# Performance work log

Hardware: AMD Instinct MI355X
Metric: run time of the kernel (lower is better)

## Reference

```python
import jax, jax.numpy as jnp
import numpy as np

N = 20000      # nodes per type
E = 320000     # edges per relation
F = 512        # raw feature dim
H = 4          # attention heads
C = 128        # hidden_channels per head
B = 64         # batch_size (num graphs)
HH = H * C
INNER = 64
NEG_SLOPE = 0.2


def _gatv2(x_src, x_dst, ei, Wl, Wr, att, b):
    """PyG GATv2Conv (concat=True, add_self_loops=True, neg_slope=0.2).
    x_src:[Ns,Fin] x_dst:[Nd,Fin'] ei:[2,E] Wl,Wr:[Fin,H*C] att:[H,C] b:[H*C].
    Returns [Nd, H*C]. Self-loop edges appended (inputs assumed loop-free)."""
    n_dst = x_dst.shape[0]
    loop = jnp.arange(min(x_src.shape[0], n_dst), dtype=ei.dtype)
    src = jnp.concatenate([ei[0], loop])
    dst = jnp.concatenate([ei[1], loop])
    xl = (x_src @ Wl).reshape(-1, H, C)   # source-side transform
    xr = (x_dst @ Wr).reshape(-1, H, C)   # target-side transform
    e = jax.nn.leaky_relu(xl[src] + xr[dst], NEG_SLOPE)   # [E',H,C]
    logit = jnp.einsum('ehc,hc->eh', e, att)               # [E',H]
    m = jax.ops.segment_max(logit, dst, num_segments=n_dst)
    m = jnp.where(jnp.isfinite(m), m, 0.0)
    p = jnp.exp(logit - m[dst])
    s = jax.ops.segment_sum(p, dst, num_segments=n_dst)
    alpha = p / jnp.maximum(s[dst], 1e-16)                 # per-dst softmax
    out = jax.ops.segment_sum(alpha[:, :, None] * xl[src], dst, num_segments=n_dst)
    return out.reshape(n_dst, HH) + b


def _layer(x_i, x_j, ei_ii, ei_jj, ei_ij, ei_ji, Wl, Wr, att, b):
    # relation order: 0:(x_i->x_i) 1:(x_j->x_j) 2:(x_i->x_j) 3:(x_j->x_i); HeteroConv aggr='sum'
    oi = _gatv2(x_i, x_i, ei_ii, Wl[0], Wr[0], att[0], b[0]) \
       + _gatv2(x_j, x_i, ei_ji, Wl[3], Wr[3], att[3], b[3])
    oj = _gatv2(x_j, x_j, ei_jj, Wl[1], Wr[1], att[1], b[1]) \
       + _gatv2(x_i, x_j, ei_ij, Wl[2], Wr[2], att[2], b[2])
    # head-sum + tanh: x.view(-1, heads, hidden).sum(1).tanh()
    oi = jnp.tanh(oi.reshape(-1, H, C).sum(axis=1))
    oj = jnp.tanh(oj.reshape(-1, H, C).sum(axis=1))
    return oi, oj


def setup_inputs() -> dict:
    key = jax.random.key(0)
    ks = jax.random.split(key, 24)
    inp = {
        'x_i': jax.random.normal(ks[0], (N, F), jnp.float32),
        'x_j': jax.random.normal(ks[1], (N, F), jnp.float32),
        'ei_ii': jax.random.randint(ks[2], (2, E), 0, N, jnp.int32),
        'ei_jj': jax.random.randint(ks[3], (2, E), 0, N, jnp.int32),
        'ei_ij': jax.random.randint(ks[4], (2, E), 0, N, jnp.int32),
        'ei_ji': jax.random.randint(ks[5], (2, E), 0, N, jnp.int32),
        'batch_i': jnp.sort(jax.random.randint(ks[6], (N,), 0, B, jnp.int32)),
        'batch_j': jnp.sort(jax.random.randint(ks[7], (N,), 0, B, jnp.int32)),
        'Wl0': jax.random.normal(ks[8], (4, F, HH), jnp.float32) / np.sqrt(F),
        'Wr0': jax.random.normal(ks[9], (4, F, HH), jnp.float32) / np.sqrt(F),
        'att0': jax.random.normal(ks[10], (4, H, C), jnp.float32) / np.sqrt(C),
        'b0': jnp.zeros((4, HH), jnp.float32),
        'Wl1': jax.random.normal(ks[11], (4, C, HH), jnp.float32) / np.sqrt(C),
        'Wr1': jax.random.normal(ks[12], (4, C, HH), jnp.float32) / np.sqrt(C),
        'att1': jax.random.normal(ks[13], (4, H, C), jnp.float32) / np.sqrt(C),
        'b1': jnp.zeros((4, HH), jnp.float32),
        'W_out': jax.random.normal(ks[14], (C, 1), jnp.float32) / np.sqrt(C),
        'b_out': jnp.zeros((1,), jnp.float32),
        'W_i': jax.random.normal(ks[15], (C, INNER), jnp.float32) / np.sqrt(C),
        'b_i': jnp.zeros((INNER,), jnp.float32),
        'W_j': jax.random.normal(ks[16], (C, INNER), jnp.float32) / np.sqrt(C),
        'b_j': jnp.zeros((INNER,), jnp.float32),
    }
    return inp


def reference(x_i, x_j, ei_ii, ei_jj, ei_ij, ei_ji, batch_i, batch_j,
              Wl0, Wr0, att0, b0, Wl1, Wr1, att1, b1,
              W_out, b_out, W_i, b_i, W_j, b_j):
    x_i, x_j = _layer(x_i, x_j, ei_ii, ei_jj, ei_ij, ei_ji, Wl0, Wr0, att0, b0)
    x_i, x_j = _layer(x_i, x_j, ei_ii, ei_jj, ei_ij, ei_ji, Wl1, Wr1, att1, b1)
    # global_add_pool per graph, then unsqueeze(1) + tanh
    p_i = jnp.tanh(jax.ops.segment_sum(x_i, batch_i, num_segments=B))[:, None, :]  # [B,1,C]
    p_j = jnp.tanh(jax.ops.segment_sum(x_j, batch_j, num_segments=B))[:, None, :]
    y_i = p_i @ W_i + b_i   # [B,1,INNER]
    y_j = p_j @ W_j + b_j
    x = (p_i + p_j)[:, 0, :]            # cat along dim=1 then sum(dim=1)
    logits = jax.nn.sigmoid(x @ W_out + b_out)   # [B,1]
    return (logits, y_i, y_j)
```

## Files before the change

kernel.cpp:

```cpp
#include <hip/hip_runtime.h>

#define NN      20000
#define EE      320000
#define ETOT    340000
#define FD      512
#define HH_     4
#define CD      128
#define HHD     512
#define BG      64
#define INNERD  64

typedef __attribute__((ext_vector_type(8))) short bf16x8;
typedef __attribute__((ext_vector_type(4))) float f32x4;

__device__ __forceinline__ float bf2f(unsigned v) { return __uint_as_float(v << 16); }
__device__ __forceinline__ unsigned short f2bf(float f) {
    unsigned u = __float_as_uint(f);
    unsigned r = 0x7fffu + ((u >> 16) & 1u);
    return (unsigned short)((u + r) >> 16);
}
__device__ __forceinline__ void load8bf(const unsigned short* p, float* f) {
    uint4 u = *reinterpret_cast<const uint4*>(p);
    f[0] = bf2f(u.x & 0xffffu); f[1] = bf2f(u.x >> 16);
    f[2] = bf2f(u.y & 0xffffu); f[3] = bf2f(u.y >> 16);
// ... 39 lines not shown
        part[t] += v;
        __syncthreads();
    }
    int run = (t > 0) ? part[t - 1] : 0;
    #pragma unroll
    for (int i = 0; i < 20; ++i) {
        int n = base + i;
        if (n < NN) { rowptr[n] = run; cursor[n] = run; run += cnt[n] + 1; }
    }
    if (t == 1023) rowptr[NN] = run;
}

__global__ __launch_bounds__(256) void csr_scatter16(const int* __restrict__ ei,
                                                     int* __restrict__ cursor,
                                                     unsigned short* __restrict__ srcs) {
    int idx = blockIdx.x * blockDim.x + threadIdx.x;
    if (idx >= ETOT) return;
    int src, dst;
    if (idx < EE) { src = ei[idx]; dst = ei[EE + idx]; }
    else          { src = dst = idx - EE; }
    int pos = atomicAdd(&cursor[dst], 1);
    srcs[pos] = (unsigned short)src;
}

__global__ __launch_bounds__(256) void csr_hist4(
    const int* __restrict__ e0, const int* __restrict__ e1,
    const int* __restrict__ e2, const int* __restrict__ e3,
    int* __restrict__ cnt)
{
    int idx = blockIdx.x * blockDim.x + threadIdx.x;
    if (idx >= 4 * EE) return;
    int r = idx / EE, e = idx - r * EE;
    const int* ei = r == 0 ? e0 : r == 1 ? e1 : r == 2 ? e2 : e3;
    atomicAdd(&cnt[r * NN + ei[EE + e]], 1);
}

__global__ __launch_bounds__(1024) void csr_scan4(const int* __restrict__ cnt_all,
                                                  int* __restrict__ rowptr_all,
                                                  int* __restrict__ cursor_all)
{
    const int r = blockIdx.x;
    const int* cnt = cnt_all + r * NN;
    int* rowptr = rowptr_all + r * (NN + 4);
    int* cursor = cursor_all + r * NN;
    __shared__ int part[1024];
    int t = threadIdx.x;
    int base = t * 20;
    int s = 0;
    #pragma unroll
    for (int i = 0; i < 20; ++i) { int n = base + i; if (n < NN) s += cnt[n] + 1; }
    part[t] = s;
    __syncthreads();
    for (int off = 1; off < 1024; off <<= 1) {
        int v = (t >= off) ? part[t - off] : 0;
        __syncthreads();
        part[t] += v;
        __syncthreads();
    }
    int run = (t > 0) ? part[t - 1] : 0;
    #pragma unroll
    for (int i = 0; i < 20; ++i) {
        int n = base + i;
        if (n < NN) { rowptr[n] = run; cursor[n] = run; run += cnt[n] + 1; }
    }
    if (t == 1023) rowptr[NN] = run;
}

__global__ __launch_bounds__(256) void csr_scatter4(
    const int* __restrict__ e0, const int* __restrict__ e1,
    const int* __restrict__ e2, const int* __restrict__ e3,
    int* __restrict__ cursor_all, unsigned short* __restrict__ srcs_all)
{
    int idx = blockIdx.x * blockDim.x + threadIdx.x;
    if (idx >= 4 * ETOT) return;
    int r = idx / ETOT, t = idx - r * ETOT;
    const int* ei = r == 0 ? e0 : r == 1 ? e1 : r == 2 ? e2 : e3;
    int src, dst;
    if (t < EE) { src = ei[t]; dst = ei[EE + t]; }
    else        { src = dst = t - EE; }
    int pos = atomicAdd(&cursor_all[r * NN + dst], 1);
    srcs_all[(size_t)r * ETOT + pos] = (unsigned short)src;
}

__global__ __launch_bounds__(256) void wsplit_t(const float* __restrict__ W,
                                                unsigned short* __restrict__ Whi,
                                                unsigned short* __restrict__ Wlo,
                                                int K)
{
    __shared__ float tile[64][65];
    const int nt = 512 / 64;
    const int kt = K / 64;
    int bid = blockIdx.x;
    int in = bid % nt; int ik = (bid / nt) % kt; int r = bid / (nt * kt);
    int t = threadIdx.x;
    const float* Wr_ = W + (size_t)r * K * 512;
    #pragma unroll
    for (int rep = 0; rep < 16; ++rep) {
        int idx = rep * 256 + t;
        int kk = idx >> 6, nn = idx & 63;
        tile[kk][nn] = Wr_[(size_t)(ik * 64 + kk) * 512 + in * 64 + nn];
    }
    __syncthreads();
    #pragma unroll
    for (int rep = 0; rep < 16; ++rep) {
        int idx = rep * 256 + t;
        int nn = idx >> 6, kk = idx & 63;
        unsigned short h, l; split_f32(tile[kk][nn], h, l);
        int n = in * 64 + nn;
        int k = ik * 64 + kk;
        size_t o = (size_t)r * 512 * K + ((size_t)(k >> 5) * 512 + n) * 32 + (k & 31);
        Whi[o] = h; Wlo[o] = l;
    }
}

template <typename TA, bool A_EXACT>
__device__ __forceinline__ void gemm_body(
    const TA* __restrict__ A, const unsigned short* __restrict__ Bhg,
    const unsigned short* __restrict__ Blg, unsigned short* __restrict__ C,
    int bx, int by, int M, int K, int N)
{
    __shared__ unsigned short Ah[128][40];
    __shared__ unsigned short Al[A_EXACT ? 1 : 128][40];

    const int tid = threadIdx.x;
    const int wave = tid >> 6, lane = tid & 63;
    const int quad = lane >> 4, lrow = lane & 15;
    const int wr = (wave >> 1) * 64, wc = (wave & 1) * 64;
    const int tileM = by * 128, tileN = bx * 128;

    const int srow = tid >> 1;
    const int sks  = (tid & 1) * 16;
    const int sgm  = tileM + srow;

    const size_t bfrag = ((size_t)(tileN + wc + lrow) << 5) + quad * 8;
    const size_t kblk  = (size_t)N << 5;

    f32x4 acc[4][4] = {};

    for (int k0 = 0; k0 < K; k0 += 32) {
        if constexpr (!A_EXACT) {
            bf16x8 ph[2] = {{}, {}}, pl[2] = {{}, {}};
            if (sgm < M) {
                const float* Ap = (const float*)A + (size_t)sgm * K + k0 + sks;
                #pragma unroll
                for (int s = 0; s < 2; ++s) {
                    float4 f0 = reinterpret_cast<const float4*>(Ap)[2 * s];
                    float4 f1 = reinterpret_cast<const float4*>(Ap)[2 * s + 1];
                    float xv[8] = {f0.x, f0.y, f0.z, f0.w, f1.x, f1.y, f1.z, f1.w};
                    #pragma unroll
                    for (int pp = 0; pp < 4; ++pp) {
                        unsigned u0 = __float_as_uint(xv[2 * pp]);
                        unsigned u1 = __float_as_uint(xv[2 * pp + 1]);
                        reinterpret_cast<unsigned*>(&ph[s])[pp] =
                            __builtin_amdgcn_perm(u1, u0, 0x07060302u);
                        float r0 = xv[2 * pp]     - __uint_as_float(u0 & 0xffff0000u);
                        float r1 = xv[2 * pp + 1] - __uint_as_float(u1 & 0xffff0000u);
                        reinterpret_cast<unsigned*>(&pl[s])[pp] =
                            __builtin_amdgcn_perm(__float_as_uint(r1), __float_as_uint(r0), 0x07060302u);
                    }
                }
            }
            *reinterpret_cast<bf16x8*>(&Ah[srow][sks])     = ph[0];
            *reinterpret_cast<bf16x8*>(&Ah[srow][sks + 8]) = ph[1];
            *reinterpret_cast<bf16x8*>(&Al[srow][sks])     = pl[0];
            *reinterpret_cast<bf16x8*>(&Al[srow][sks + 8]) = pl[1];
        } else {
            bf16x8 v0 = {}, v1 = {};
            if (sgm < M) {
                const unsigned short* Ap = (const unsigned short*)A + (size_t)sgm * K + k0 + sks;
                v0 = reinterpret_cast<const bf16x8*>(Ap)[0];
                v1 = reinterpret_cast<const bf16x8*>(Ap)[1];
            }
            *reinterpret_cast<bf16x8*>(&Ah[srow][sks])     = v0;
            *reinterpret_cast<bf16x8*>(&Ah[srow][sks + 8]) = v1;
        }
        bf16x8 bh[4], bl[4];
        {
            const unsigned short* Bb = Bhg + (size_t)(k0 >> 5) * kblk + bfrag;
            const unsigned short* Bc = Blg + (size_t)(k0 >> 5) * kblk + bfrag;
            #pragma unroll
            for (int ni = 0; ni < 4; ++ni) {
                bh[ni] = *reinterpret_cast<const bf16x8*>(Bb + ((size_t)ni << 9));
                bl[ni] = *reinterpret_cast<const bf16x8*>(Bc + ((size_t)ni << 9));
            }
        }
        __syncthreads();
        bf16x8 ah[4], al[4];
        #pragma unroll
        for (int mi = 0; mi < 4; ++mi) {
            ah[mi] = *reinterpret_cast<const bf16x8*>(&Ah[wr + mi * 16 + lrow][quad * 8]);
            if constexpr (!A_EXACT)
                al[mi] = *reinterpret_cast<const bf16x8*>(&Al[wr + mi * 16 + lrow][quad * 8]);
        }
        #pragma unroll
        for (int mi = 0; mi < 4; ++mi)
// ... 445 lines not shown
        size_t ai = (size_t)dst * CD + lane * 8;
        if (add_in) {
            #pragma unroll
            for (int j = 0; j < 8; ++j) o[j] += acc[ai + j];
        }
        if (fin_mode == 0) {
            #pragma unroll
            for (int j = 0; j < 8; ++j) acc[ai + j] = o[j];
        } else {
            int c0 = lane * 8;
            #pragma unroll
            for (int j = 0; j < 8; ++j) {
                float bb = 0.f;
                #pragma unroll
                for (int h = 0; h < HH_; ++h)
                    bb += bA[h * CD + c0 + j] + bB[h * CD + c0 + j];
                o[j] = tanhf(o[j] + bb);
            }
            if (fin_mode == 1) {
                #pragma unroll
                for (int j = 0; j < 8; ++j) z[ai + j] = f2bf(o[j]);
            } else {
                #pragma unroll
                for (int j = 0; j < 8; ++j) acc[ai + j] = o[j];
            }
        }
    }
}

__global__ __launch_bounds__(256) void fused_aggr4d(
    const int* __restrict__ rp0, const unsigned short* __restrict__ sr0,
    const unsigned short* __restrict__ xl0, const unsigned short* __restrict__ xr0,
    const float* __restrict__ attA,
    const int* __restrict__ rp1, const unsigned short* __restrict__ sr1,
    const unsigned short* __restrict__ xl1, const unsigned short* __restrict__ xr1,
    const float* __restrict__ attB,
    float* __restrict__ acc, int fin_mode,
    const float* __restrict__ bA, const float* __restrict__ bB,
    unsigned short* __restrict__ z,
    const int* __restrict__ batch, float* __restrict__ pool)
{
    int dst = (int)((blockIdx.x * (size_t)blockDim.x + threadIdx.x) >> 6);
    int lane = threadIdx.x & 63;
    if (dst >= NN) return;
    aggr4d_body(dst, lane, rp0, sr0, xl0, xr0, attA, rp1, sr1, xl1, xr1, attB,
                acc, fin_mode, bA, bB, z);
}

__global__ __launch_bounds__(256) void fused_aggr4d_pair(
    const int* __restrict__ irp0, const unsigned short* __restrict__ isr0,
    const unsigned short* __restrict__ ixl0, const unsigned short* __restrict__ ixr0,
    const float* __restrict__ iattA,
    const int* __restrict__ irp1, const unsigned short* __restrict__ isr1,
    const unsigned short* __restrict__ ixl1, const unsigned short* __restrict__ ixr1,
    const float* __restrict__ iattB,
    float* __restrict__ accA,
    const float* __restrict__ ibA, const float* __restrict__ ibB,
    const int* __restrict__ jrp0, const unsigned short* __restrict__ jsr0,
    const unsigned short* __restrict__ jxl0, const unsigned short* __restrict__ jxr0,
    const float* __restrict__ jattA,
    const int* __restrict__ jrp1, const unsigned short* __restrict__ jsr1,
    const unsigned short* __restrict__ jxl1, const unsigned short* __restrict__ jxr1,
    const float* __restrict__ jattB,
    float* __restrict__ accB,
    const float* __restrict__ jbA, const float* __restrict__ jbB)
{
    const int half = NN / 4;
    int lane = threadIdx.x & 63;
    if ((int)blockIdx.x < half) {
        int dst = (int)((blockIdx.x * (size_t)blockDim.x + threadIdx.x) >> 6);
        if (dst >= NN) return;
        aggr4d_body(dst, lane, irp0, isr0, ixl0, ixr0, iattA,
                    irp1, isr1, ixl1, ixr1, iattB, accA, 2, ibA, ibB, nullptr);
    } else {
        int dst = (int)(((blockIdx.x - half) * (size_t)blockDim.x + threadIdx.x) >> 6);
        if (dst >= NN) return;
        aggr4d_body(dst, lane, jrp0, jsr0, jxl0, jxr0, jattA,
                    jrp1, jsr1, jxl1, jxr1, jattB, accB, 2, jbA, jbB, nullptr);
    }
}

template <typename TA, bool A_EXACT>
__global__ __launch_bounds__(256, 3) void gemm_aggr_fused(
    int ngemm,
    const TA* __restrict__ A0, const TA* __restrict__ A1,
    const TA* __restrict__ A2, const TA* __restrict__ A3,
    const unsigned short* __restrict__ B0h, const unsigned short* __restrict__ B0l,
    const unsigned short* __restrict__ B1h, const unsigned short* __restrict__ B1l,
    const unsigned short* __restrict__ B2h, const unsigned short* __restrict__ B2l,
    const unsigned short* __restrict__ B3h, const unsigned short* __restrict__ B3l,
    unsigned short* __restrict__ C0, unsigned short* __restrict__ C1,
    unsigned short* __restrict__ C2, unsigned short* __restrict__ C3,
    int M, int K, int N,
    const int* __restrict__ rp0, const unsigned short* __restrict__ sr0,
    const unsigned short* __restrict__ xl0, const unsigned short* __restrict__ xr0,
    const float* __restrict__ attA,
    const int* __restrict__ rp1, const unsigned short* __restrict__ sr1,
    const unsigned short* __restrict__ xl1, const unsigned short* __restrict__ xr1,
    const float* __restrict__ attB,
    float* __restrict__ acc, int fin_mode,
    const float* __restrict__ bA, const float* __restrict__ bB,
    unsigned short* __restrict__ zout)
{
    if ((int)blockIdx.x < ngemm) {
        int b = blockIdx.x;
        int xcd = b & 7, q8 = ngemm >> 3, r8 = ngemm & 7;
        int work = (xcd < r8 ? xcd * (q8 + 1) : r8 * (q8 + 1) + (xcd - r8) * q8) + (b >> 3);
        const int gx = N / 128, gy = (M + 127) / 128;
        int bx = work % gx; int t2 = work / gx; int by = t2 % gy; int bz = t2 / gy;
        const TA* A = bz == 0 ? A0 : bz == 1 ? A1 : bz == 2 ? A2 : A3;
        const unsigned short* Bh = bz == 0 ? B0h : bz == 1 ? B1h : bz == 2 ? B2h : B3h;
        const unsigned short* Bl = bz == 0 ? B0l : bz == 1 ? B1l : bz == 2 ? B2l : B3l;
        unsigned short* C = bz == 0 ? C0 : bz == 1 ? C1 : bz == 2 ? C2 : C3;
        gemm_body<TA, A_EXACT>(A, Bh, Bl, C, bx, by, M, K, N);
    } else {
        int dst = (int)(((blockIdx.x - ngemm) * (size_t)blockDim.x + threadIdx.x) >> 6);
        int lane = threadIdx.x & 63;
        if (dst >= NN) return;
        aggr4d_body(dst, lane, rp0, sr0, xl0, xr0, attA, rp1, sr1, xl1, xr1, attB,
                    acc, fin_mode, bA, bB, zout);
    }
}

__global__ __launch_bounds__(512) void pool_reduce(
    const float* __restrict__ acc, const int* __restrict__ batch,
    float* __restrict__ pool)
{
    int b = blockIdx.x;
    int t = threadIdx.x & (CD - 1);
    int q = threadIdx.x >> 7;
    int lo, hi;
    { int l = 0, r = NN; while (l < r) { int m = (l + r) >> 1; if (batch[m] < b) l = m + 1; else r = m; } lo = l; }
    { int l = lo, r = NN; while (l < r) { int m = (l + r) >> 1; if (batch[m] <= b) l = m + 1; else r = m; } hi = l; }
    float s = 0.f;
    for (int nrow = lo + q; nrow < hi; nrow += 4)
        s += acc[(size_t)nrow * CD + t];
    __shared__ float red[4][CD];
    red[q][t] = s;
    __syncthreads();
    if (q == 0)
        pool[(size_t)b * CD + t] = red[0][t] + red[1][t] + red[2][t] + red[3][t];
}

__global__ __launch_bounds__(512) void pool_reduce2(
    const float* __restrict__ accA, const int* __restrict__ batchA, float* __restrict__ poolA,
    const float* __restrict__ accB, const int* __restrict__ batchB, float* __restrict__ poolB)
{
    int g = blockIdx.x;
    const float* acc = (g < BG) ? accA : accB;
    const int* batch = (g < BG) ? batchA : batchB;
    float* pool = (g < BG) ? poolA : poolB;
    int b = (g < BG) ? g : g - BG;
    int t = threadIdx.x & (CD - 1);
    int q = threadIdx.x >> 7;
    int lo, hi;
    { int l = 0, r = NN; while (l < r) { int m = (l + r) >> 1; if (batch[m] < b) l = m + 1; else r = m; } lo = l; }
    { int l = lo, r = NN; while (l < r) { int m = (l + r) >> 1; if (batch[m] <= b) l = m + 1; else r = m; } hi = l; }
    float s = 0.f;
    for (int nrow = lo + q; nrow < hi; nrow += 4)
        s += acc[(size_t)nrow * CD + t];
    __shared__ float red[4][CD];
    red[q][t] = s;
    __syncthreads();
    if (q == 0)
        pool[(size_t)b * CD + t] = red[0][t] + red[1][t] + red[2][t] + red[3][t];
}

__global__ __launch_bounds__(128) void head_kernel(
    const float* __restrict__ pool_i, const float* __restrict__ pool_j,
    const float* __restrict__ W_out, const float* __restrict__ b_out,
    const float* __restrict__ W_i, const float* __restrict__ b_i,
    const float* __restrict__ W_j, const float* __restrict__ b_j,
    float* __restrict__ out)
{
    int b = blockIdx.x;
    int t = threadIdx.x;
    __shared__ float pi[CD], pj[CD];
    pi[t] = tanhf(pool_i[(size_t)b * CD + t]);
    pj[t] = tanhf(pool_j[(size_t)b * CD + t]);
    __syncthreads();
    if (t < INNERD) {
        float a = b_i[t];
        for (int c = 0; c < CD; ++c) a += pi[c] * W_i[c * INNERD + t];
        out[BG + (size_t)b * INNERD + t] = a;
    } else {
        int k = t - INNERD;
        float a = b_j[k];
        for (int c = 0; c < CD; ++c) a += pj[c] * W_j[c * INNERD + k];
        out[BG + BG * INNERD + (size_t)b * INNERD + k] = a;
    }
    if (t == 0) {
        float a = b_out[0];
        for (int c = 0; c < CD; ++c) a += (pi[c] + pj[c]) * W_out[c];
        out[b] = 1.f / (1.f + expf(-a));
    }
}

struct Ws {
    unsigned short *xl, *xr, *xl2, *xr2, *xl3, *xr3, *xl4, *xr4, *z_i, *z_j;
// ... 140 lines not shown
    const int* batch_j = (const int*)d_in[7];
    const float* Wl0   = (const float*)d_in[8];
    const float* Wr0   = (const float*)d_in[9];
    const float* att0  = (const float*)d_in[10];
    const float* b0    = (const float*)d_in[11];
    const float* Wl1   = (const float*)d_in[12];
    const float* Wr1   = (const float*)d_in[13];
    const float* att1  = (const float*)d_in[14];
    const float* b1    = (const float*)d_in[15];
    const float* W_out = (const float*)d_in[16];
    const float* b_out = (const float*)d_in[17];
    const float* W_i   = (const float*)d_in[18];
    const float* b_i   = (const float*)d_in[19];
    const float* W_j   = (const float*)d_in[20];
    const float* b_j   = (const float*)d_in[21];
    float* out = (float*)d_out;

    const size_t FAT2_BYTES = (size_t)NN * HHD * 2 * 2 + (size_t)NN * CD * 4
                            + (size_t)NN * CD * 2 * 2 + 4 * (size_t)ETOT * 2
                            + 4 * (size_t)(NN + 4) * 4 + 4 * (size_t)NN * 4 * 2
                            + (size_t)BG * CD * 4 * 2;
    const size_t FAT1_BYTES = (size_t)NN * HHD * 2 * 2 + (size_t)NN * CD * 4
                            + (size_t)NN * CD * 2 * 2 + (size_t)ETOT * 2
                            + (size_t)(NN + 4) * 4 + (size_t)NN * 4 * 2
                            + (size_t)BG * CD * 4 * 2;
    const size_t WT0_ONE = (size_t)4 * 512 * 512 * 2;
    const size_t WT1_ONE = (size_t)4 * 512 * 128 * 2;
    const size_t WT_BYTES = 4 * WT0_ONE + 4 * WT1_ONE;
    const size_t X2_BYTES = 2 * (size_t)NN * HHD * 2;
    const size_t ACC2_BYTES = (size_t)NN * CD * 4;

    const int ncsr = (ws_size >= FAT2_BYTES) ? 4 : 1;
    const bool fat = (ws_size >= FAT1_BYTES);
    const bool fat_t = (ws_size >= FAT2_BYTES + WT_BYTES);
    const bool fat_m = (ws_size >= FAT2_BYTES + WT_BYTES + X2_BYTES);
    const bool fat_f = (ws_size >= FAT2_BYTES + WT_BYTES + 3 * X2_BYTES);
    const bool fat_g = (ws_size >= FAT2_BYTES + WT_BYTES + 3 * X2_BYTES + ACC2_BYTES);

    Ws w;
    char* p = (char*)d_ws;
    size_t xbytes = fat ? (size_t)NN * HHD * 2 : (size_t)NN * CD * 2;
    w.xl     = (unsigned short*)p; p += xbytes;
    w.xr     = (unsigned short*)p; p += xbytes;
    w.acc    = (float*)p;          p += (size_t)NN * CD * 4;
    w.z_i    = (unsigned short*)p; p += (size_t)NN * CD * 2;
    w.z_j    = (unsigned short*)p; p += (size_t)NN * CD * 2;
    {
        int* rowptr_all = (int*)p;            p += (size_t)ncsr * (NN + 4) * 4;
        unsigned short* srcs_all = (unsigned short*)p; p += (size_t)ncsr * ETOT * 2;
        for (int r = 0; r < 4; ++r) {
            int rr = (r < ncsr) ? r : 0;
            w.rowptr[r] = rowptr_all + (size_t)rr * (NN + 4);
            w.srcs[r]   = srcs_all + (size_t)rr * ETOT;
        }
    }
    w.cnt    = (int*)p;            p += (size_t)ncsr * NN * 4;
    w.cursor = (int*)p;            p += (size_t)ncsr * NN * 4;
    w.pool_i = (float*)p;          p += (size_t)BG * CD * 4;
    w.pool_j = (float*)p;          p += (size_t)BG * CD * 4;
    if (fat_t) {
        w.wt0l_h = (unsigned short*)p; p += WT0_ONE;
        w.wt0l_l = (unsigned short*)p; p += WT0_ONE;
        w.wt0r_h = (unsigned short*)p; p += WT0_ONE;
        w.wt0r_l = (unsigned short*)p; p += WT0_ONE;
        w.wt1l_h = (unsigned short*)p; p += WT1_ONE;
        w.wt1l_l = (unsigned short*)p; p += WT1_ONE;
        w.wt1r_h = (unsigned short*)p; p += WT1_ONE;
        w.wt1r_l = (unsigned short*)p; p += WT1_ONE;
    }
    if (fat_m) {
        w.xl2 = (unsigned short*)p; p += (size_t)NN * HHD * 2;
        w.xr2 = (unsigned short*)p; p += (size_t)NN * HHD * 2;
    }
    if (fat_f) {
        w.xl3 = (unsigned short*)p; p += (size_t)NN * HHD * 2;
        w.xr3 = (unsigned short*)p; p += (size_t)NN * HHD * 2;
        w.xl4 = (unsigned short*)p; p += (size_t)NN * HHD * 2;
        w.xr4 = (unsigned short*)p; p += (size_t)NN * HHD * 2;
    }
    if (fat_g) {
        w.acc2 = (float*)p; p += ACC2_BYTES;
    }

    hipMemsetAsync(w.pool_i, 0, (size_t)BG * CD * sizeof(float), stream);
    hipMemsetAsync(w.pool_j, 0, (size_t)BG * CD * sizeof(float), stream);

    const int* eis_all[4] = { ei_ii, ei_jj, ei_ij, ei_ji };
    const float* srcA0_i[2] = { x_i, x_j };  const float* dstA0_i[2] = { x_i, x_i };
    const float* srcA0_j[2] = { x_j, x_i };  const float* dstA0_j[2] = { x_j, x_j };
    const int rids_i[2] = { 0, 3 };
    const int rids_j[2] = { 1, 2 };
    const unsigned short* srcA1_i[2] = { w.z_i, w.z_j };
    const unsigned short* dstA1_i[2] = { w.z_i, w.z_i };
    const unsigned short* srcA1_j[2] = { w.z_j, w.z_i };
    const unsigned short* dstA1_j[2] = { w.z_j, w.z_j };

    if (fat_t) {
        hipMemsetAsync(w.cnt, 0, 4 * NN * sizeof(int), stream);
        csr_hist4<<<(4 * EE + 255) / 256, 256, 0, stream>>>(
            ei_ii, ei_jj, ei_ij, ei_ji, w.cnt);
        csr_scan4<<<4, 1024, 0, stream>>>(w.cnt, w.rowptr[0], w.cursor);
        csr_scatter4<<<(4 * ETOT + 255) / 256, 256, 0, stream>>>(
            ei_ii, ei_jj, ei_ij, ei_ji, w.cursor, w.srcs[0]);
        wsplit_t<<<4 * (FD / 64) * 8, 256, 0, stream>>>(Wl0, w.wt0l_h, w.wt0l_l, FD);
        wsplit_t<<<4 * (FD / 64) * 8, 256, 0, stream>>>(Wr0, w.wt0r_h, w.wt0r_l, FD);
        wsplit_t<<<4 * (CD / 64) * 8, 256, 0, stream>>>(Wl1, w.wt1l_h, w.wt1l_l, CD);
        wsplit_t<<<4 * (CD / 64) * 8, 256, 0, stream>>>(Wr1, w.wt1r_h, w.wt1r_l, CD);

        const int* rp_i[2] = { w.rowptr[0], w.rowptr[3] };
        const unsigned short* sr_i[2] = { w.srcs[0], w.srcs[3] };
        const int* rp_j[2] = { w.rowptr[1], w.rowptr[2] };
        const unsigned short* sr_j[2] = { w.srcs[1], w.srcs[2] };

        if (fat_g) {
            const size_t o0 = (size_t)0 * HHD * FD, o3 = (size_t)3 * HHD * FD;
            const size_t o1 = (size_t)1 * HHD * FD, o2 = (size_t)2 * HHD * FD;
            const size_t p0 = (size_t)0 * HHD * CD, p1 = (size_t)1 * HHD * CD;
            const size_t p2 = (size_t)2 * HHD * CD, p3 = (size_t)3 * HHD * CD;
            dim3 gg(HHD / 128, (NN + 127) / 128, 4);
            gemm_mfma_t4<float, false><<<gg, 256, 0, stream>>>(
                x_i, x_i, x_j, x_i,
                w.wt0l_h + o0, w.wt0l_l + o0, w.wt0r_h + o0, w.wt0r_l + o0,
                w.wt0l_h + o3, w.wt0l_l + o3, w.wt0r_h + o3, w.wt0r_l + o3,
                w.xl, w.xr, w.xl2, w.xr2, NN, FD, HHD);
            const int ngemm0 = (HHD / 128) * ((NN + 127) / 128) * 4;
            gemm_aggr_fused<float, false><<<ngemm0 + NN / 4, 256, 0, stream>>>(
                ngemm0,
                x_j, x_j, x_i, x_j,
                w.wt0l_h + o1, w.wt0l_l + o1, w.wt0r_h + o1, w.wt0r_l + o1,
                w.wt0l_h + o2, w.wt0l_l + o2, w.wt0r_h + o2, w.wt0r_l + o2,
                w.xl3, w.xr3, w.xl4, w.xr4, NN, FD, HHD,
                w.rowptr[0], w.srcs[0], w.xl, w.xr, att0 + (size_t)0 * HHD,
                w.rowptr[3], w.srcs[3], w.xl2, w.xr2, att0 + (size_t)3 * HHD,
                w.acc, 1, b0 + (size_t)0 * HHD, b0 + (size_t)3 * HHD, w.z_i);
            gemm_aggr_fused<unsigned short, true><<<ngemm0 + NN / 4, 256, 0, stream>>>(
                ngemm0,
                w.z_i, w.z_i, w.z_i, w.z_i,
                w.wt1l_h + p0, w.wt1l_l + p0, w.wt1r_h + p0, w.wt1r_l + p0,
                w.wt1r_h + p3, w.wt1r_l + p3, w.wt1l_h + p2, w.wt1l_l + p2,
                w.xl, w.xr, w.xr2, w.xl2, NN, CD, HHD,
                w.rowptr[1], w.srcs[1], w.xl3, w.xr3, att0 + (size_t)1 * HHD,
                w.rowptr[2], w.srcs[2], w.xl4, w.xr4, att0 + (size_t)2 * HHD,
                w.acc, 1, b0 + (size_t)1 * HHD, b0 + (size_t)2 * HHD, w.z_j);
            gemm_mfma_t4<unsigned short, true><<<gg, 256, 0, stream>>>(
                w.z_j, w.z_j, w.z_j, w.z_j,
                w.wt1l_h + p3, w.wt1l_l + p3, w.wt1l_h + p1, w.wt1l_l + p1,
                w.wt1r_h + p1, w.wt1r_l + p1, w.wt1r_h + p2, w.wt1r_l + p2,
                w.xl4, w.xl3, w.xr3, w.xr4, NN, CD, HHD);
            fused_aggr4d_pair<<<2 * (NN / 4), 256, 0, stream>>>(
                w.rowptr[0], w.srcs[0], w.xl, w.xr, att1 + (size_t)0 * HHD,
                w.rowptr[3], w.srcs[3], w.xl4, w.xr2, att1 + (size_t)3 * HHD,
                w.acc, b1 + (size_t)0 * HHD, b1 + (size_t)3 * HHD,
                w.rowptr[1], w.srcs[1], w.xl3, w.xr3, att1 + (size_t)1 * HHD,
                w.rowptr[2], w.srcs[2], w.xl2, w.xr4, att1 + (size_t)2 * HHD,
                w.acc2, b1 + (size_t)1 * HHD, b1 + (size_t)2 * HHD);
            pool_reduce2<<<2 * BG, 512, 0, stream>>>(
                w.acc, batch_i, w.pool_i, w.acc2, batch_j, w.pool_j);
        } else if (fat_f) {
            const size_t o0 = (size_t)0 * HHD * FD, o3 = (size_t)3 * HHD * FD;
            const size_t o1 = (size_t)1 * HHD * FD, o2 = (size_t)2 * HHD * FD;
            dim3 gg(HHD / 128, (NN + 127) / 128, 4);
            gemm_mfma_t4<float, false><<<gg, 256, 0, stream>>>(
                x_i, x_i, x_j, x_i,
                w.wt0l_h + o0, w.wt0l_l + o0, w.wt0r_h + o0, w.wt0r_l + o0,
                w.wt0l_h + o3, w.wt0l_l + o3, w.wt0r_h + o3, w.wt0r_l + o3,
                w.xl, w.xr, w.xl2, w.xr2, NN, FD, HHD);
            const int ngemm = (HHD / 128) * ((NN + 127) / 128) * 4;
            gemm_aggr_fused<float, false><<<ngemm + NN / 4, 256, 0, stream>>>(
                ngemm,
                x_j, x_j, x_i, x_j,
                w.wt0l_h + o1, w.wt0l_l + o1, w.wt0r_h + o1, w.wt0r_l + o1,
                w.wt0l_h + o2, w.wt0l_l + o2, w.wt0r_h + o2, w.wt0r_l + o2,
                w.xl3, w.xr3, w.xl4, w.xr4, NN, FD, HHD,
                w.rowptr[0], w.srcs[0], w.xl, w.xr, att0 + (size_t)0 * HHD,
                w.rowptr[3], w.srcs[3], w.xl2, w.xr2, att0 + (size_t)3 * HHD,
                w.acc, 1, b0 + (size_t)0 * HHD, b0 + (size_t)3 * HHD, w.z_i);
            fused_aggr4d<<<NN / 4, 256, 0, stream>>>(
                w.rowptr[1], w.srcs[1], w.xl3, w.xr3, att0 + (size_t)1 * HHD,
                w.rowptr[2], w.srcs[2], w.xl4, w.xr4, att0 + (size_t)2 * HHD,
                w.acc, 1, b0 + (size_t)1 * HHD, b0 + (size_t)2 * HHD,
                w.z_j, nullptr, nullptr);
            dim3 g8(HHD / 128, (NN + 127) / 128, 8);
            gemm_mfma_L1x8<<<g8, 256, 0, stream>>>(
                w.z_i, w.z_j, w.wt1l_h, w.wt1l_l, w.wt1r_h, w.wt1r_l,
                w.xl, w.xr, w.xl2, w.xr2, w.xl3, w.xr3, w.xl4, w.xr4,
                NN, CD, HHD);
            fused_aggr4d<<<NN / 4, 256, 0, stream>>>(
                w.rowptr[0], w.srcs[0], w.xl, w.xr, att1 + (size_t)0 * HHD,
                w.rowptr[3], w.srcs[3], w.xl2, w.xr2, att1 + (size_t)3 * HHD,
                w.acc, 2, b1 + (size_t)0 * HHD, b1 + (size_t)3 * HHD,
                nullptr, nullptr, nullptr);
            pool_reduce<<<BG, 512, 0, stream>>>(w.acc, batch_i, w.pool_i);
            fused_aggr4d<<<NN / 4, 256, 0, stream>>>(
                w.rowptr[1], w.srcs[1], w.xl3, w.xr3, att1 + (size_t)1 * HHD,
                w.rowptr[2], w.srcs[2], w.xl4, w.xr4, att1 + (size_t)2 * HHD,
                w.acc, 2, b1 + (size_t)1 * HHD, b1 + (size_t)2 * HHD,
                nullptr, nullptr, nullptr);
            pool_reduce<<<BG, 512, 0, stream>>>(w.acc, batch_j, w.pool_j);
        } else if (fat_m) {
            run_group_fat_m<float, false>(srcA0_i, dstA0_i, rp_i, sr_i, rids_i, FD,
                                          w.wt0l_h, w.wt0l_l, w.wt0r_h, w.wt0r_l,
                                          att0, b0, 1, w.z_i, nullptr, nullptr, w, stream);
            run_group_fat_m<float, false>(srcA0_j, dstA0_j, rp_j, sr_j, rids_j, FD,
                                          w.wt0l_h, w.wt0l_l, w.wt0r_h, w.wt0r_l,
                                          att0, b0, 1, w.z_j, nullptr, nullptr, w, stream);
            run_group_fat_m<unsigned short, true>(srcA1_i, dstA1_i, rp_i, sr_i, rids_i, CD,
                                                  w.wt1l_h, w.wt1l_l, w.wt1r_h, w.wt1r_l,
                                                  att1, b1, 2, nullptr, batch_i, w.pool_i, w, stream);
            pool_reduce<<<BG, 512, 0, stream>>>(w.acc, batch_i, w.pool_i);
            run_group_fat_m<unsigned short, true>(srcA1_j, dstA1_j, rp_j, sr_j, rids_j, CD,
                                                  w.wt1l_h, w.wt1l_l, w.wt1r_h, w.wt1r_l,
                                                  att1, b1, 2, nullptr, batch_j, w.pool_j, w, stream);
            pool_reduce<<<BG, 512, 0, stream>>>(w.acc, batch_j, w.pool_j);
        } else {
            run_group_fat_t<float, false>(srcA0_i, dstA0_i, rp_i, sr_i, rids_i, FD,
                                          w.wt0l_h, w.wt0l_l, w.wt0r_h, w.wt0r_l,
                                          att0, b0, 1, w.z_i, nullptr, nullptr, w, stream);
            run_group_fat_t<float, false>(srcA0_j, dstA0_j, rp_j, sr_j, rids_j, FD,
                                          w.wt0l_h, w.wt0l_l, w.wt0r_h, w.wt0r_l,
                                          att0, b0, 1, w.z_j, nullptr, nullptr, w, stream);
            run_group_fat_t<unsigned short, true>(srcA1_i, dstA1_i, rp_i, sr_i, rids_i, CD,
                                                  w.wt1l_h, w.wt1l_l, w.wt1r_h, w.wt1r_l,
                                                  att1, b1, 2, nullptr, batch_i, w.pool_i, w, stream);
            pool_reduce<<<BG, 512, 0, stream>>>(w.acc, batch_i, w.pool_i);
            run_group_fat_t<unsigned short, true>(srcA1_j, dstA1_j, rp_j, sr_j, rids_j, CD,
                                                  w.wt1l_h, w.wt1l_l, w.wt1r_h, w.wt1r_l,
                                                  att1, b1, 2, nullptr, batch_j, w.pool_j, w, stream);
            pool_reduce<<<BG, 512, 0, stream>>>(w.acc, batch_j, w.pool_j);
        }
    } else if (fat) {
        if (ncsr == 4) {
            for (int r = 0; r < 4; ++r)
                build_csr(eis_all[r], w.rowptr[r], w.srcs[r], w.cnt, w.cursor, stream);
            const int* rp_i[2] = { w.rowptr[0], w.rowptr[3] };
            const unsigned short* sr_i[2] = { w.srcs[0], w.srcs[3] };
            const int* rp_j[2] = { w.rowptr[1], w.rowptr[2] };
            const unsigned short* sr_j[2] = { w.srcs[1], w.srcs[2] };
            run_group_fat<float, false>(srcA0_i, dstA0_i, rp_i, sr_i, rids_i, FD,
                                        Wl0, Wr0, att0, b0, 1, w.z_i, nullptr, nullptr, w, stream);
            run_group_fat<float, false>(srcA0_j, dstA0_j, rp_j, sr_j, rids_j, FD,
                                        Wl0, Wr0, att0, b0, 1, w.z_j, nullptr, nullptr, w, stream);
            run_group_fat<unsigned short, true>(srcA1_i, dstA1_i, rp_i, sr_i, rids_i, CD,
                                                Wl1, Wr1, att1, b1, 2, nullptr, batch_i, w.pool_i, w, stream);
            pool_reduce<<<BG, 512, 0, stream>>>(w.acc, batch_i, w.pool_i);
            run_group_fat<unsigned short, true>(srcA1_j, dstA1_j, rp_j, sr_j, rids_j, CD,
                                                Wl1, Wr1, att1, b1, 2, nullptr, batch_j, w.pool_j, w, stream);
            pool_reduce<<<BG, 512, 0, stream>>>(w.acc, batch_j, w.pool_j);
        } else {
            for (int pass = 0; pass < 4; ++pass) {
                const int* rids = (pass & 1) ? rids_j : rids_i;
                for (int q = 0; q < 2; ++q) {
                    int r = rids[q];
// ... 50 lines not shown
```

Baseline: 1.237 ms.

## Interleave GEMM and aggregation blocks in fused kernel; merge weight-split launches

The fused GEMM+aggregation kernel now spreads GEMM tiles evenly across the block index range instead of putting all GEMM blocks first. Each block decides its role from a proportional mapping, so aggregation and GEMM blocks are co-resident and compute-bound and memory-bound work can overlap. The four weight-split launches are merged into one kernel, and the pool memsets are skipped on the fat path, where they appear to be unused. The interleaving may change cache locality and the XCD-aware tile assignment for the GEMM blocks.

Result: no change. 1.249 ms (+0.9%).

```diff
diff --git a/kernel.cpp b/kernel.cpp
--- a/kernel.cpp
+++ b/kernel.cpp
@@ -145,16 +145,14 @@
     srcs_all[(size_t)r * ETOT + pos] = (unsigned short)src;
 }
 
-__global__ __launch_bounds__(256) void wsplit_t(const float* __restrict__ W,
-                                                unsigned short* __restrict__ Whi,
-                                                unsigned short* __restrict__ Wlo,
-                                                int K)
+__device__ __forceinline__ void wsplit_body(const float* __restrict__ W,
+                                            unsigned short* __restrict__ Whi,
+                                            unsigned short* __restrict__ Wlo,
+                                            int K, int bid)
 {
     __shared__ float tile[64][65];
     const int nt = 512 / 64;
-    const int kt = K / 64;
-    int bid = blockIdx.x;
-    int in = bid % nt; int ik = (bid / nt) % kt; int r = bid / (nt * kt);
+    int in = bid % nt; int ik = (bid / nt) % (K / 64); int r = bid / (nt * (K / 64));
     int t = threadIdx.x;
     const float* Wr_ = W + (size_t)r * K * 512;
     #pragma unroll
@@ -174,6 +172,21 @@
         size_t o = (size_t)r * 512 * K + ((size_t)(k >> 5) * 512 + n) * 32 + (k & 31);
         Whi[o] = h; Wlo[o] = l;
     }
+}
+
+__global__ __launch_bounds__(256) void wsplit_all(
+    const float* __restrict__ Wl0, const float* __restrict__ Wr0,
+    const float* __restrict__ Wl1, const float* __restrict__ Wr1,
+    unsigned short* __restrict__ w0lh, unsigned short* __restrict__ w0ll,
+    unsigned short* __restrict__ w0rh, unsigned short* __restrict__ w0rl,
+    unsigned short* __restrict__ w1lh, unsigned short* __restrict__ w1ll,
+    unsigned short* __restrict__ w1rh, unsigned short* __restrict__ w1rl)
+{
+    int b = blockIdx.x;
+    if (b < 256)      wsplit_body(Wl0, w0lh, w0ll, FD, b);
+    else if (b < 512) wsplit_body(Wr0, w0rh, w0rl, FD, b - 256);
+    else if (b < 576) wsplit_body(Wl1, w1lh, w1ll, CD, b - 512);
+    else              wsplit_body(Wr1, w1rh, w1rl, CD, b - 576);
 }
 
 template <typename TA, bool A_EXACT>
@@ -785,7 +798,7 @@
 
 template <typename TA, bool A_EXACT>
 __global__ __launch_bounds__(256, 3) void gemm_aggr_fused(
-    int ngemm,
+    int ngemm, int ntot,
     const TA* __restrict__ A0, const TA* __restrict__ A1,
     const TA* __restrict__ A2, const TA* __restrict__ A3,
     const unsigned short* __restrict__ B0h, const unsigned short* __restrict__ B0l,
@@ -805,10 +818,13 @@
     const float* __restrict__ bA, const float* __restrict__ bB,
     unsigned short* __restrict__ zout)
 {
-    if ((int)blockIdx.x < ngemm) {
-        int b = blockIdx.x;
-        int xcd = b & 7, q8 = ngemm >> 3, r8 = ngemm & 7;
-        int work = (xcd < r8 ? xcd * (q8 + 1) : r8 * (q8 + 1) + (xcd - r8) * q8) + (b >> 3);
+    int b = (int)blockIdx.x;
+    int cb = (int)(((long long)b * ngemm) / ntot);
+    bool is_gemm = ((int)(((long long)(b + 1) * ngemm) / ntot) > cb);
+    if (is_gemm) {
+        int g = cb;
+        int xcd = g & 7, q8 = ngemm >> 3, r8 = ngemm & 7;
+        int work = (xcd < r8 ? xcd * (q8 + 1) : r8 * (q8 + 1) + (xcd - r8) * q8) + (g >> 3);
         const int gx = N / 128, gy = (M + 127) / 128;
         int bx = work % gx; int t2 = work / gx; int by = t2 % gy; int bz = t2 / gy;
         const TA* A = bz == 0 ? A0 : bz == 1 ? A1 : bz == 2 ? A2 : A3;
@@ -817,7 +833,8 @@
         unsigned short* C = bz == 0 ? C0 : bz == 1 ? C1 : bz == 2 ? C2 : C3;
         gemm_body<TA, A_EXACT>(A, Bh, Bl, C, bx, by, M, K, N);
     } else {
-        int dst = (int)(((blockIdx.x - ngemm) * (size_t)blockDim.x + threadIdx.x) >> 6);
+        int ab = b - cb;
+        int dst = (int)(((size_t)ab * blockDim.x + threadIdx.x) >> 6);
         int lane = threadIdx.x & 63;
         if (dst >= NN) return;
         aggr4d_body(dst, lane, rp0, sr0, xl0, xr0, attA, rp1, sr1, xl1, xr1, attB,
@@ -1124,8 +1141,10 @@
         w.acc2 = (float*)p; p += ACC2_BYTES;
     }
 
-    hipMemsetAsync(w.pool_i, 0, (size_t)BG * CD * sizeof(float), stream);
-    hipMemsetAsync(w.pool_j, 0, (size_t)BG * CD * sizeof(float), stream);
+    if (!fat) {
+        hipMemsetAsync(w.pool_i, 0, (size_t)BG * CD * sizeof(float), stream);
+        hipMemsetAsync(w.pool_j, 0, (size_t)BG * CD * sizeof(float), stream);
+    }
 
     const int* eis_all[4] = { ei_ii, ei_jj, ei_ij, ei_ji };
     const float* srcA0_i[2] = { x_i, x_j };  const float* dstA0_i[2] = { x_i, x_i };
@@ -1144,10 +1163,10 @@
         csr_scan4<<<4, 1024, 0, stream>>>(w.cnt, w.rowptr[0], w.cursor);
         csr_scatter4<<<(4 * ETOT + 255) / 256, 256, 0, stream>>>(
             ei_ii, ei_jj, ei_ij, ei_ji, w.cursor, w.srcs[0]);
-        wsplit_t<<<4 * (FD / 64) * 8, 256, 0, stream>>>(Wl0, w.wt0l_h, w.wt0l_l, FD);
-        wsplit_t<<<4 * (FD / 64) * 8, 256, 0, stream>>>(Wr0, w.wt0r_h, w.wt0r_l, FD);
-        wsplit_t<<<4 * (CD / 64) * 8, 256, 0, stream>>>(Wl1, w.wt1l_h, w.wt1l_l, CD);
-        wsplit_t<<<4 * (CD / 64) * 8, 256, 0, stream>>>(Wr1, w.wt1r_h, w.wt1r_l, CD);
+        wsplit_all<<<640, 256, 0, stream>>>(
+            Wl0, Wr0, Wl1, Wr1,
+            w.wt0l_h, w.wt0l_l, w.wt0r_h, w.wt0r_l,
+            w.wt1l_h, w.wt1l_l, w.wt1r_h, w.wt1r_l);
 
         const int* rp_i[2] = { w.rowptr[0], w.rowptr[3] };
         const unsigned short* sr_i[2] = { w.srcs[0], w.srcs[3] };
@@ -1166,8 +1185,9 @@
                 w.wt0l_h + o3, w.wt0l_l + o3, w.wt0r_h + o3, w.wt0r_l + o3,
                 w.xl, w.xr, w.xl2, w.xr2, NN, FD, HHD);
             const int ngemm0 = (HHD / 128) * ((NN + 127) / 128) * 4;
-            gemm_aggr_fused<float, false><<<ngemm0 + NN / 4, 256, 0, stream>>>(
-                ngemm0,
+            const int ntot0 = ngemm0 + NN / 4;
+            gemm_aggr_fused<float, false><<<ntot0, 256, 0, stream>>>(
+                ngemm0, ntot0,
                 x_j, x_j, x_i, x_j,
                 w.wt0l_h + o1, w.wt0l_l + o1, w.wt0r_h + o1, w.wt0r_l + o1,
                 w.wt0l_h + o2, w.wt0l_l + o2, w.wt0r_h + o2, w.wt0r_l + o2,
@@ -1175,8 +1195,8 @@
                 w.rowptr[0], w.srcs[0], w.xl, w.xr, att0 + (size_t)0 * HHD,
                 w.rowptr[3], w.srcs[3], w.xl2, w.xr2, att0 + (size_t)3 * HHD,
                 w.acc, 1, b0 + (size_t)0 * HHD, b0 + (size_t)3 * HHD, w.z_i);
-            gemm_aggr_fused<unsigned short, true><<<ngemm0 + NN / 4, 256, 0, stream>>>(
-                ngemm0,
+            gemm_aggr_fused<unsigned short, true><<<ntot0, 256, 0, stream>>>(
+                ngemm0, ntot0,
                 w.z_i, w.z_i, w.z_i, w.z_i,
                 w.wt1l_h + p0, w.wt1l_l + p0, w.wt1r_h + p0, w.wt1r_l + p0,
                 w.wt1r_h + p3, w.wt1r_l + p3, w.wt1l_h + p2, w.wt1l_l + p2,
@@ -1208,8 +1228,9 @@
                 w.wt0l_h + o3, w.wt0l_l + o3, w.wt0r_h + o3, w.wt0r_l + o3,
                 w.xl, w.xr, w.xl2, w.xr2, NN, FD, HHD);
             const int ngemm = (HHD / 128) * ((NN + 127) / 128) * 4;
-            gemm_aggr_fused<float, false><<<ngemm + NN / 4, 256, 0, stream>>>(
-                ngemm,
+            const int ntot = ngemm + NN / 4;
+            gemm_aggr_fused<float, false><<<ntot, 256, 0, stream>>>(
+                ngemm, ntot,
                 x_j, x_j, x_i, x_j,
                 w.wt0l_h + o1, w.wt0l_l + o1, w.wt0r_h + o1, w.wt0r_l + o1,
                 w.wt0l_h + o2, w.wt0l_l + o2, w.wt0r_h + o2, w.wt0r_l + o2,
```
